# Performance work log

Hardware: AMD Instinct MI355X
Metric: run time of the kernel (lower is better)

The kernel has to match this reference:

```python
import jax, jax.numpy as jnp
import numpy as np

N_NODES = 50000
N_EDGES = 800000
IN_F, HID_F, OUT_F = 256, 128, 64
NEG_SLOPE = 0.2
EPS = 1e-16


def _aggregate_with_attention(x, src, tgt, a_w, a_b, num_nodes):
    # x: [N, d]; src/tgt: [E]; a_w: [2d]; a_b: [1]
    d = x.shape[-1]
    x_src = x[src]                                   # [E, d] gather
    # att(cat([x_src, x_tgt])) == x_src @ a_w[:d] + x_tgt @ a_w[d:] + b
    alpha = x_src @ a_w[:d] + x[tgt] @ a_w[d:] + a_b[0]   # [E]
    alpha = jnp.where(alpha >= 0, alpha, NEG_SLOPE * alpha)  # leaky_relu(0.2)
    # segment softmax over edges grouped by target node
    m = jax.ops.segment_max(alpha, tgt, num_segments=num_nodes)   # [N]
    e = jnp.exp(alpha - m[tgt])                                    # [E]
    s = jax.ops.segment_sum(e, tgt, num_segments=num_nodes)       # [N]
    alpha = e / (s[tgt] + EPS)                                     # [E]
    msgs = x_src * alpha[:, None]                                  # [E, d]
    return jax.ops.segment_sum(msgs, tgt, num_segments=num_nodes)  # [N, d]


def setup_inputs() -> dict:
    key = jax.random.key(0)
    ks = jax.random.split(key, 10)
    x = jax.random.normal(ks[0], (N_NODES, IN_F), dtype=jnp.float32)
    edge_index = jax.random.randint(ks[1], (2, N_EDGES), 0, N_NODES, dtype=jnp.int32)
    sc1 = 1.0 / np.sqrt(IN_F)
    sc2 = 1.0 / np.sqrt(HID_F)
    return {
        "x": x,
        "edge_index": edge_index,
        "W1": jax.random.normal(ks[2], (IN_F, HID_F), dtype=jnp.float32) * sc1,
        "b1": jax.random.normal(ks[3], (HID_F,), dtype=jnp.float32) * sc1,
        "a1_w": jax.random.normal(ks[4], (2 * HID_F,), dtype=jnp.float32) * sc2,
        "a1_b": jax.random.normal(ks[5], (1,), dtype=jnp.float32) * sc2,
        "W2": jax.random.normal(ks[6], (HID_F, OUT_F), dtype=jnp.float32) * sc2,
        "b2": jax.random.normal(ks[7], (OUT_F,), dtype=jnp.float32) * sc2,
        "a2_w": jax.random.normal(ks[8], (2 * OUT_F,), dtype=jnp.float32) * (1.0 / np.sqrt(OUT_F)),
        "a2_b": jax.random.normal(ks[9], (1,), dtype=jnp.float32) * (1.0 / np.sqrt(OUT_F)),
    }


def reference(x, edge_index, W1, b1, a1_w, a1_b, W2, b2, a2_w, a2_b):
    src, tgt = edge_index[0], edge_index[1]
    n = x.shape[0]
    # eval mode: dropout is identity
    h = jax.nn.elu(x @ W1 + b1)                           # [N, HID]
    h = _aggregate_with_attention(h, src, tgt, a1_w, a1_b, n)
    o = h @ W2 + b2                                        # [N, OUT]
    o = _aggregate_with_attention(o, src, tgt, a2_w, a2_b, n)
    return jax.nn.log_softmax(o, axis=-1)
```

## Files before the change

kernel.cpp:

```cpp
#include <hip/hip_runtime.h>

#define NN    50000
#define NE    800000
#define INF_  256
#define HIDF  128
#define OUTF  64
#define NBUCK 196
#define CAP   5120
#define CHUNK 2048
#define NPART1 ((NE + CHUNK - 1) / CHUNK)
#define NLIN1  ((NN + 63) / 64)
#define NPREP  160

typedef unsigned int uint;
typedef unsigned short ushort;
typedef __attribute__((ext_vector_type(8))) short short8;
typedef __attribute__((ext_vector_type(4))) float float4v;

__device__ __forceinline__ short f2bf(float f) {
    union { float f; unsigned u; } v; v.f = f;
    unsigned r = v.u + 0x7fffu + ((v.u >> 16) & 1u);
    return (short)(r >> 16);
}
__device__ __forceinline__ float bflo(uint u) {
    union { uint u; float f; } v; v.u = u << 16; return v.f;
}
__device__ __forceinline__ float bfhi(uint u) {
    union { uint u; float f; } v; v.u = u & 0xffff0000u; return v.f;
}

__device__ __forceinline__ int excl_scan256(int v, int* ws) {
    int lane = threadIdx.x & 63, wv = threadIdx.x >> 6;
    int x = v;
    #pragma unroll
    for (int o = 1; o < 64; o <<= 1) {
        int y = __shfl_up(x, o);
        if (lane >= o) x += y;
    }
    if (lane == 63) ws[wv] = x;
    __syncthreads();
    int add = 0;
    #pragma unroll
    for (int w = 0; w < 4; w++) add += (w < wv) ? ws[w] : 0;
    return x + add - v;
}

__global__ __launch_bounds__(256) void k_prep(const float* __restrict__ W1, const float* __restrict__ W2,
                                              short* __restrict__ W1f, short* __restrict__ W2f,
                                              int* __restrict__ bcur) {
    if (blockIdx.x == NPREP) {
        if (threadIdx.x < NBUCK) bcur[threadIdx.x] = 0;
        return;
    }
    int i = blockIdx.x * 256 + threadIdx.x;
    if (i < INF_ * HIDF) {
        int kk = i & 7, t = i >> 3;
        int m_l = t & 15, q = (t >> 4) & 3, s = t >> 6;
        int nb = s & 7, kc = s >> 3;
        int k = kc * 32 + q * 8 + kk, n = nb * 16 + m_l;
        W1f[i] = f2bf(W1[k * HIDF + n]);
    } else if (i < INF_ * HIDF + HIDF * OUTF) {
        int i2 = i - INF_ * HIDF;
        int kk = i2 & 7, t = i2 >> 3;
        int m_l = t & 15, q = (t >> 4) & 3, s = t >> 6;
        int nb = s & 3, kc = s >> 2;
        int k = kc * 32 + q * 8 + kk, n = nb * 16 + m_l;
        W2f[i2] = f2bf(W2[k * OUTF + n]);
    }
}


__global__ __launch_bounds__(256, 3) void k_f1(const int* __restrict__ src, const int* __restrict__ tgt,
                                               int* __restrict__ bcur, uint2* __restrict__ pairs,
                                               const float* __restrict__ X, const short* __restrict__ W1f,
                                               const float* __restrict__ b1, ushort* __restrict__ Hb,
                                               const float* __restrict__ a1w, float* __restrict__ s1s,
                                               float* __restrict__ s1t) {
    if (blockIdx.x < NPART1) {
        __shared__ int hist[NBUCK], lofs[NBUCK], cur[NBUCK], gstart[NBUCK];
        __shared__ int ws[4];
        __shared__ int ltgt[CHUNK], lsrc[CHUNK];
        int tid = threadIdx.x;
        for (int i = tid; i < NBUCK; i += 256) hist[i] = 0;
        __syncthreads();

        int base = blockIdx.x * CHUNK;
        int cnt = NE - base; if (cnt > CHUNK) cnt = CHUNK;

        int t_[8], s_[8];
        #pragma unroll
        for (int k = 0; k < 8; k++) {
            int idx = k * 256 + tid;
            if (idx < cnt) {
                int j = base + idx;
                t_[k] = tgt[j]; s_[k] = src[j];
                atomicAdd(&hist[t_[k] >> 8], 1);
            } else t_[k] = -1;
        }
        __syncthreads();

        int v = (tid < NBUCK) ? hist[tid] : 0;
        int excl = excl_scan256(v, ws);
        if (tid < NBUCK) {
            lofs[tid] = excl;
            cur[tid] = excl;
            gstart[tid] = atomicAdd(&bcur[tid], v);
        }
        __syncthreads();

        #pragma unroll
        for (int k = 0; k < 8; k++) {
            if (t_[k] >= 0) {
                int b = t_[k] >> 8;
                int pos = atomicAdd(&cur[b], 1);
                ltgt[pos] = t_[k]; lsrc[pos] = s_[k];
            }
        }
        __syncthreads();

        for (int j = tid; j < cnt; j += 256) {
            int tv = ltgt[j];
            int b = tv >> 8;
            int dst = gstart[b] + (j - lofs[b]);
            pairs[(size_t)b * CAP + dst] = make_uint2((uint)tv, (uint)lsrc[j]);
        }
        return;
    }
    int bid = blockIdx.x - NPART1;
    int w = threadIdx.x >> 6;
    int l = threadIdx.x & 63;
    int m_l = l & 15, q = l >> 4;
    int row0 = bid * 64 + w * 16;
    int rA0 = row0 + m_l;
    int rc0 = rA0 < NN ? rA0 : NN - 1;
    const float* pa0 = X + (size_t)rc0 * INF_ + q * 8;
    const short8* Bp = (const short8*)W1f;

    float4 xu[16];
    #pragma unroll
    for (int kc = 0; kc < 8; kc++) {
        xu[2 * kc]     = *(const float4*)(pa0 + kc * 32);
        xu[2 * kc + 1] = *(const float4*)(pa0 + kc * 32 + 4);
    }
    short8 af[8];
    #pragma unroll
    for (int kc = 0; kc < 8; kc++) {
        float4 u0 = xu[2 * kc], u1 = xu[2 * kc + 1];
        af[kc][0] = f2bf(u0.x); af[kc][1] = f2bf(u0.y); af[kc][2] = f2bf(u0.z); af[kc][3] = f2bf(u0.w);
        af[kc][4] = f2bf(u1.x); af[kc][5] = f2bf(u1.y); af[kc][6] = f2bf(u1.z); af[kc][7] = f2bf(u1.w);
    }

    float4v acc[8] = {};
    #pragma unroll
    for (int kc = 0; kc < 8; kc++) {
        #pragma unroll
        for (int n = 0; n < 8; n++) {
            short8 b = Bp[(kc * 8 + n) * 64 + l];
            acc[n] = __builtin_amdgcn_mfma_f32_16x16x32_bf16(af[kc], b, acc[n], 0, 0, 0);
        }
    }

    float vs_r[4] = {0.f, 0.f, 0.f, 0.f}, vt_r[4] = {0.f, 0.f, 0.f, 0.f};
    #pragma unroll
    for (int n = 0; n < 8; n++) {
        int col = n * 16 + m_l;
        float bias = b1[col];
        float aw0 = a1w[col], aw1 = a1w[HIDF + col];
        #pragma unroll
        for (int r = 0; r < 4; r++) {
            int row = row0 + q * 4 + r;
            float v = acc[n][r] + bias;
            v = v > 0.f ? v : expm1f(v);
            vs_r[r] += v * aw0; vt_r[r] += v * aw1;
            if (row < NN) Hb[(size_t)row * HIDF + col] = (ushort)f2bf(v);
        }
    }
    #pragma unroll
    for (int r = 0; r < 4; r++) {
        #pragma unroll
        for (int o = 1; o < 16; o <<= 1) {
            vs_r[r] += __shfl_xor(vs_r[r], o);
            vt_r[r] += __shfl_xor(vt_r[r], o);
        }
    }
    if (m_l == 0) {
        #pragma unroll
        for (int r = 0; r < 4; r++) {
            int row = row0 + q * 4 + r;
            if (row < NN) { s1s[row] = vs_r[r]; s1t[row] = vt_r[r]; }
        }
    }
}

__global__ __launch_bounds__(256) void k_part2(const int* __restrict__ bcur, const uint2* __restrict__ pairs,
                                               int* __restrict__ fsrc, int* __restrict__ nbeg,
                                               int* __restrict__ ncnt) {
    __shared__ int hist[256], cur[256];
    __shared__ int ws[4];
    int tid = threadIdx.x;
    int b = blockIdx.x;
    int cnt = __builtin_amdgcn_readfirstlane(bcur[b]);
    hist[tid] = 0;
    __syncthreads();

    const uint2* pb = pairs + (size_t)b * CAP;
    for (int j = tid; j < cnt; j += 256) {
        uint2 e = pb[j];
        atomicAdd(&hist[e.x & 255], 1);
    }
    __syncthreads();

    int v = hist[tid];
    int excl = excl_scan256(v, ws);
    int node = (b << 8) + tid;
    if (node < NN) { nbeg[node] = b * CAP + excl; ncnt[node] = v; }
    cur[tid] = excl;
    __syncthreads();

    for (int j = tid; j < cnt; j += 256) {
        uint2 e = pb[j];
        int pos = atomicAdd(&cur[e.x & 255], 1);
        fsrc[(size_t)b * CAP + pos] = (int)e.y;
    }
}

__global__ __launch_bounds__(256, 3) void k_linear2(const short* __restrict__ Hin, const short* __restrict__ W2f,
                                                    const float* __restrict__ b2, ushort* __restrict__ Ob,
                                                    const float* __restrict__ a2w, float* __restrict__ s2s,
                                                    float* __restrict__ s2t) {
    int w = threadIdx.x >> 6;
    int l = threadIdx.x & 63;
    int m_l = l & 15, q = l >> 4;
    int row0 = blockIdx.x * 64 + w * 16;
    int rA0 = row0 + m_l;
    int rc0 = rA0 < NN ? rA0 : NN - 1;
    const short* pa0 = Hin + (size_t)rc0 * HIDF + q * 8;
    const short8* Bp = (const short8*)W2f;

    short8 af[4];
    #pragma unroll
    for (int kc = 0; kc < 4; kc++) af[kc] = *(const short8*)(pa0 + kc * 32);

    float4v acc[4] = {};
    #pragma unroll
    for (int kc = 0; kc < 4; kc++) {
        #pragma unroll
        for (int n = 0; n < 4; n++) {
            short8 b = Bp[(kc * 4 + n) * 64 + l];
            acc[n] = __builtin_amdgcn_mfma_f32_16x16x32_bf16(af[kc], b, acc[n], 0, 0, 0);
        }
    }

    float vs_r[4] = {0.f, 0.f, 0.f, 0.f}, vt_r[4] = {0.f, 0.f, 0.f, 0.f};
    #pragma unroll
    for (int n = 0; n < 4; n++) {
        int col = n * 16 + m_l;
        float bias = b2[col];
        float aw0 = a2w[col], aw1 = a2w[OUTF + col];
        #pragma unroll
        for (int r = 0; r < 4; r++) {
            int row = row0 + q * 4 + r;
            float v = acc[n][r] + bias;
            vs_r[r] += v * aw0; vt_r[r] += v * aw1;
            if (row < NN) Ob[(size_t)row * OUTF + col] = (ushort)f2bf(v);
        }
    }
    #pragma unroll
    for (int r = 0; r < 4; r++) {
        #pragma unroll
        for (int o = 1; o < 16; o <<= 1) {
            vs_r[r] += __shfl_xor(vs_r[r], o);
            vt_r[r] += __shfl_xor(vt_r[r], o);
        }
    }
    if (m_l == 0) {
        #pragma unroll
        for (int r = 0; r < 4; r++) {
            int row = row0 + q * 4 + r;
            if (row < NN) { s2s[row] = vs_r[r]; s2t[row] = vt_r[r]; }
        }
    }
}


__global__ __launch_bounds__(256) void k_agg1f(const uint* __restrict__ Hb4, const int* __restrict__ nbeg,
                                               const int* __restrict__ ncnt, const int* __restrict__ fsrc,
                                               const float* __restrict__ ss, const float* __restrict__ st_,
                                               const float* __restrict__ ab, uint* __restrict__ Hagg4) {
    int wid  = (blockIdx.x * 256 + threadIdx.x) >> 6;
    int lane = threadIdx.x & 63;
    if (wid >= NN) return;
    int beg = __builtin_amdgcn_readfirstlane(nbeg[wid]);
    int deg = __builtin_amdgcn_readfirstlane(ncnt[wid]);
    int end = beg + deg;
    float bias = ab[0] + st_[wid];
    float ax = 0.f, ay = 0.f, bx = 0.f, by = 0.f;

    if (deg > 0 && deg <= 64) {
        int my_s = 0; float a = -INFINITY;
        if (lane < deg) {
            my_s = fsrc[beg + lane];
            float t = ss[my_s] + bias;
            a = t >= 0.f ? t : 0.2f * t;
        }
        float m = a;
        #pragma unroll
        for (int o = 32; o > 0; o >>= 1) m = fmaxf(m, __shfl_xor(m, o));
        float e = (lane < deg) ? __expf(a - m) : 0.f;
        float sum = e;
        #pragma unroll
        for (int o = 32; o > 0; o >>= 1) sum += __shfl_xor(sum, o);
        float p = e * (1.f / (sum + 1e-16f));
        for (int j = 0; j < deg; j += 8) {
            int sA[8]; float wA[8]; uint xA[8];
            #pragma unroll
            for (int u = 0; u < 8; u++) { sA[u] = __shfl(my_s, j + u); wA[u] = __shfl(p, j + u); }
            #pragma unroll
            for (int u = 0; u < 8; u++) xA[u] = Hb4[(size_t)sA[u] * 64 + lane];
            #pragma unroll
            for (int u = 0; u < 8; u += 2) {
                ax += wA[u] * bflo(xA[u]);         ay += wA[u] * bfhi(xA[u]);
                bx += wA[u + 1] * bflo(xA[u + 1]); by += wA[u + 1] * bfhi(xA[u + 1]);
            }
        }
    } else if (deg > 64) {
        float m = -INFINITY;
        for (int i = beg + lane; i < end; i += 64) {
            float t = ss[fsrc[i]] + bias;
            t = t >= 0.f ? t : 0.2f * t;
            m = fmaxf(m, t);
        }
        #pragma unroll
        for (int o = 32; o > 0; o >>= 1) m = fmaxf(m, __shfl_xor(m, o));
        float sum = 0.f;
        for (int i = beg + lane; i < end; i += 64) {
            float t = ss[fsrc[i]] + bias;
            t = t >= 0.f ? t : 0.2f * t;
            sum += __expf(t - m);
        }
        #pragma unroll
        for (int o = 32; o > 0; o >>= 1) sum += __shfl_xor(sum, o);
        float inv = 1.f / (sum + 1e-16f);
        for (int c = beg; c < end; c += 64) {
            int cnt = min(64, end - c);
            int my_s = 0; float p = 0.f;
            if (lane < cnt) {
                my_s = fsrc[c + lane];
                float t = ss[my_s] + bias;
                t = t >= 0.f ? t : 0.2f * t;
                p = __expf(t - m) * inv;
            }
            for (int j = 0; j < cnt; j += 4) {
                int s0 = __shfl(my_s, j),     s1 = __shfl(my_s, j + 1);
                int s2 = __shfl(my_s, j + 2), s3 = __shfl(my_s, j + 3);
                float w0 = __shfl(p, j),     w1 = __shfl(p, j + 1);
                float w2 = __shfl(p, j + 2), w3 = __shfl(p, j + 3);
                uint x0 = Hb4[(size_t)s0 * 64 + lane];
                uint x1 = Hb4[(size_t)s1 * 64 + lane];
                uint x2 = Hb4[(size_t)s2 * 64 + lane];
                uint x3 = Hb4[(size_t)s3 * 64 + lane];
                ax += w0 * bflo(x0); ay += w0 * bfhi(x0);
                bx += w1 * bflo(x1); by += w1 * bfhi(x1);
                ax += w2 * bflo(x2); ay += w2 * bfhi(x2);
                bx += w3 * bflo(x3); by += w3 * bfhi(x3);
            }
        }
    }
    float fx = ax + bx, fy = ay + by;
    uint outv = (uint)(ushort)f2bf(fx) | ((uint)(ushort)f2bf(fy) << 16);
    Hagg4[(size_t)wid * 64 + lane] = outv;
}

__global__ __launch_bounds__(256) void k_agg2f(const uint* __restrict__ Ob4, const int* __restrict__ nbeg,
                                               const int* __restrict__ ncnt, const int* __restrict__ fsrc,
                                               const float* __restrict__ ss, const float* __restrict__ st_,
                                               const float* __restrict__ ab, float* __restrict__ out) {
    int wid  = (blockIdx.x * 256 + threadIdx.x) >> 6;
    int lane = threadIdx.x & 63;
    if (wid >= NN) return;
    int half = lane >> 5, li = lane & 31;
    int beg = __builtin_amdgcn_readfirstlane(nbeg[wid]);
    int deg = __builtin_amdgcn_readfirstlane(ncnt[wid]);
    int end = beg + deg;
    float bias = ab[0] + st_[wid];
    float a0 = 0.f, a1 = 0.f;

    if (deg > 0 && deg <= 64) {
        int my_s = 0; float a = -INFINITY;
        if (lane < deg) {
            my_s = fsrc[beg + lane];
            float t = ss[my_s] + bias;
            a = t >= 0.f ? t : 0.2f * t;
        }
        float m = a;
        #pragma unroll
        for (int o = 32; o > 0; o >>= 1) m = fmaxf(m, __shfl_xor(m, o));
        float e = (lane < deg) ? __expf(a - m) : 0.f;
        float sum = e;
        #pragma unroll
        for (int o = 32; o > 0; o >>= 1) sum += __shfl_xor(sum, o);
        float p = e * (1.f / (sum + 1e-16f));
        for (int j = 0; j < deg; j += 8) {
            int e0 = j + half, e1 = j + 2 + half, e2 = j + 4 + half, e3 = j + 6 + half;
            int s0 = __shfl(my_s, e0), s1 = __shfl(my_s, e1);
            int s2 = __shfl(my_s, e2), s3 = __shfl(my_s, e3);
            float w0 = __shfl(p, e0), w1 = __shfl(p, e1);
            float w2 = __shfl(p, e2), w3 = __shfl(p, e3);
            uint x0 = Ob4[(size_t)s0 * 32 + li];
            uint x1 = Ob4[(size_t)s1 * 32 + li];
            uint x2 = Ob4[(size_t)s2 * 32 + li];
            uint x3 = Ob4[(size_t)s3 * 32 + li];
            a0 += w0 * bflo(x0); a1 += w0 * bfhi(x0);
            a0 += w1 * bflo(x1); a1 += w1 * bfhi(x1);
            a0 += w2 * bflo(x2); a1 += w2 * bfhi(x2);
            a0 += w3 * bflo(x3); a1 += w3 * bfhi(x3);
        }
    } else if (deg > 64) {
        float m = -INFINITY;
        for (int i = beg + lane; i < end; i += 64) {
            float t = ss[fsrc[i]] + bias;
            t = t >= 0.f ? t : 0.2f * t;
            m = fmaxf(m, t);
        }
        #pragma unroll
        for (int o = 32; o > 0; o >>= 1) m = fmaxf(m, __shfl_xor(m, o));
        float sum = 0.f;
        for (int i = beg + lane; i < end; i += 64) {
            float t = ss[fsrc[i]] + bias;
            t = t >= 0.f ? t : 0.2f * t;
            sum += __expf(t - m);
        }
        #pragma unroll
        for (int o = 32; o > 0; o >>= 1) sum += __shfl_xor(sum, o);
        float inv = 1.f / (sum + 1e-16f);
        for (int c = beg; c < end; c += 64) {
            int cnt = min(64, end - c);
            int my_s = 0; float p = 0.f;
            if (lane < cnt) {
                my_s = fsrc[c + lane];
                float t = ss[my_s] + bias;
                t = t >= 0.f ? t : 0.2f * t;
                p = __expf(t - m) * inv;
            }
            for (int j = 0; j < cnt; j += 4) {
                int e0 = j + half, e1 = j + 2 + half;
                int s0 = __shfl(my_s, e0), s1 = __shfl(my_s, e1);
                float w0 = __shfl(p, e0), w1 = __shfl(p, e1);
                uint x0 = Ob4[(size_t)s0 * 32 + li];
                uint x1 = Ob4[(size_t)s1 * 32 + li];
                a0 += w0 * bflo(x0); a1 += w0 * bfhi(x0);
                a0 += w1 * bflo(x1); a1 += w1 * bfhi(x1);
            }
        }
    }
    a0 += __shfl_xor(a0, 32);
    a1 += __shfl_xor(a1, 32);
    float mx = fmaxf(a0, a1);
    #pragma unroll
    for (int o = 16; o > 0; o >>= 1) mx = fmaxf(mx, __shfl_xor(mx, o));
    float es = __expf(a0 - mx) + __expf(a1 - mx);
    #pragma unroll
    for (int o = 16; o > 0; o >>= 1) es += __shfl_xor(es, o);
    float lg = __logf(es);
    if (half == 0) {
        float2 r; r.x = a0 - mx - lg; r.y = a1 - mx - lg;
        ((float2*)out)[(size_t)wid * 32 + li] = r;
    }
}


extern "C" void kernel_launch(void* const* d_in, const int* in_sizes, int n_in,
                              void* d_out, int out_size, void* d_ws, size_t ws_size,
                              hipStream_t stream) {
    const float* X   = (const float*)d_in[0];
    const int*   ei  = (const int*)d_in[1];
    const float* W1  = (const float*)d_in[2];
    const float* b1  = (const float*)d_in[3];
    const float* a1w = (const float*)d_in[4];
    const float* a1b = (const float*)d_in[5];
    const float* W2  = (const float*)d_in[6];
    const float* b2  = (const float*)d_in[7];
    const float* a2w = (const float*)d_in[8];
    const float* a2b = (const float*)d_in[9];
    const int* src = ei;
    const int* tgt = ei + NE;

    char* p = (char*)d_ws;
    size_t off = 0;
    auto alloc = [&](size_t bytes) -> char* {
        char* r = p + off;
        off = (off + bytes + 255) & ~(size_t)255;
        return r;
    };
    ushort* Hb    = (ushort*)alloc((size_t)NN * HIDF * 2);
    ushort* Hagg  = (ushort*)alloc((size_t)NN * HIDF * 2);
    ushort* Ob    = (ushort*)alloc((size_t)NN * OUTF * 2);
    short* W1f    = (short*)alloc((size_t)INF_ * HIDF * 2);
    short* W2f    = (short*)alloc((size_t)HIDF * OUTF * 2);
    float* s1s    = (float*)alloc((size_t)NN * 4);
    float* s1t    = (float*)alloc((size_t)NN * 4);
    float* s2s    = (float*)alloc((size_t)NN * 4);
    float* s2t    = (float*)alloc((size_t)NN * 4);
    int*   bcur   = (int*)alloc((size_t)NBUCK * 4);
    uint2* pairs  = (uint2*)alloc((size_t)NBUCK * CAP * 8);
    int*   fsrc   = (int*)alloc((size_t)NBUCK * CAP * 4);
    int*   nbeg   = (int*)alloc((size_t)NN * 4);
    int*   ncnt   = (int*)alloc((size_t)NN * 4);

    k_prep   <<<NPREP + 1, 256, 0, stream>>>(W1, W2, W1f, W2f, bcur);
    k_f1     <<<NPART1 + NLIN1, 256, 0, stream>>>(src, tgt, bcur, pairs,
                                                  X, W1f, b1, Hb, a1w, s1s, s1t);
    k_part2  <<<NBUCK, 256, 0, stream>>>(bcur, pairs, fsrc, nbeg, ncnt);
    k_agg1f  <<<NN / 4, 256, 0, stream>>>((const uint*)Hb, nbeg, ncnt, fsrc, s1s, s1t, a1b, (uint*)Hagg);
    k_linear2<<<NLIN1, 256, 0, stream>>>((const short*)Hagg, W2f, b2, Ob, a2w, s2s, s2t);
    k_agg2f  <<<NN / 4, 256, 0, stream>>>((const uint*)Ob, nbeg, ncnt, fsrc, s2s, s2t, a2b, (float*)d_out);
}
```

Before: 212.0 us.

## Stage X tile through LDS as bf16 and widen gather unroll to 16

The linear-layer part of k_f1 now loads the 64-row X tile with coalesced float4 reads, converts it to bf16 and stores it in padded shared memory (unioned with the partition scratch). MFMA A-fragments are then read from LDS instead of being held as 64 floats of strided global loads per lane. This aims to improve load coalescing and cut register pressure, and the launch_bounds occupancy hint is dropped. Separately, the aggregation loop for low-degree nodes gathers 16 neighbours per iteration instead of 8 to keep more loads in flight, at the cost of more registers and extra shuffles for padded lanes.

```diff
diff --git a/kernel.cpp b/kernel.cpp
--- a/kernel.cpp
+++ b/kernel.cpp
@@ -11,6 +11,7 @@
 #define NPART1 ((NE + CHUNK - 1) / CHUNK)
 #define NLIN1  ((NN + 63) / 64)
 #define NPREP  160
+#define XLD   264
 
 typedef unsigned int uint;
 typedef unsigned short ushort;
@@ -70,18 +71,26 @@
 }
 
 
-__global__ __launch_bounds__(256, 3) void k_f1(const int* __restrict__ src, const int* __restrict__ tgt,
-                                               int* __restrict__ bcur, uint2* __restrict__ pairs,
-                                               const float* __restrict__ X, const short* __restrict__ W1f,
-                                               const float* __restrict__ b1, ushort* __restrict__ Hb,
-                                               const float* __restrict__ a1w, float* __restrict__ s1s,
-                                               float* __restrict__ s1t) {
+struct P1Mem {
+    int hist[NBUCK], lofs[NBUCK], cur[NBUCK], gstart[NBUCK];
+    int ws[4];
+    int ltgt[CHUNK], lsrc[CHUNK];
+};
+union SMem {
+    P1Mem p1;
+    ushort xs[64][XLD];
+};
+
+__global__ __launch_bounds__(256) void k_f1(const int* __restrict__ src, const int* __restrict__ tgt,
+                                            int* __restrict__ bcur, uint2* __restrict__ pairs,
+                                            const float* __restrict__ X, const short* __restrict__ W1f,
+                                            const float* __restrict__ b1, ushort* __restrict__ Hb,
+                                            const float* __restrict__ a1w, float* __restrict__ s1s,
+                                            float* __restrict__ s1t) {
+    __shared__ SMem sm;
     if (blockIdx.x < NPART1) {
-        __shared__ int hist[NBUCK], lofs[NBUCK], cur[NBUCK], gstart[NBUCK];
-        __shared__ int ws[4];
-        __shared__ int ltgt[CHUNK], lsrc[CHUNK];
         int tid = threadIdx.x;
-        for (int i = tid; i < NBUCK; i += 256) hist[i] = 0;
+        for (int i = tid; i < NBUCK; i += 256) sm.p1.hist[i] = 0;
         __syncthreads();
 
         int base = blockIdx.x * CHUNK;
@@ -94,17 +103,17 @@
             if (idx < cnt) {
                 int j = base + idx;
                 t_[k] = tgt[j]; s_[k] = src[j];
-                atomicAdd(&hist[t_[k] >> 8], 1);
+                atomicAdd(&sm.p1.hist[t_[k] >> 8], 1);
             } else t_[k] = -1;
         }
         __syncthreads();
 
-        int v = (tid < NBUCK) ? hist[tid] : 0;
-        int excl = excl_scan256(v, ws);
+        int v = (tid < NBUCK) ? sm.p1.hist[tid] : 0;
+        int excl = excl_scan256(v, sm.p1.ws);
         if (tid < NBUCK) {
-            lofs[tid] = excl;
-            cur[tid] = excl;
-            gstart[tid] = atomicAdd(&bcur[tid], v);
+            sm.p1.lofs[tid] = excl;
+            sm.p1.cur[tid] = excl;
+            sm.p1.gstart[tid] = atomicAdd(&bcur[tid], v);
         }
         __syncthreads();
 
@@ -112,51 +121,52 @@
         for (int k = 0; k < 8; k++) {
             if (t_[k] >= 0) {
                 int b = t_[k] >> 8;
-                int pos = atomicAdd(&cur[b], 1);
-                ltgt[pos] = t_[k]; lsrc[pos] = s_[k];
+                int pos = atomicAdd(&sm.p1.cur[b], 1);
+                sm.p1.ltgt[pos] = t_[k]; sm.p1.lsrc[pos] = s_[k];
             }
         }
         __syncthreads();
 
         for (int j = tid; j < cnt; j += 256) {
-            int tv = ltgt[j];
+            int tv = sm.p1.ltgt[j];
             int b = tv >> 8;
-            int dst = gstart[b] + (j - lofs[b]);
-            pairs[(size_t)b * CAP + dst] = make_uint2((uint)tv, (uint)lsrc[j]);
+            int dst = sm.p1.gstart[b] + (j - sm.p1.lofs[b]);
+            pairs[(size_t)b * CAP + dst] = make_uint2((uint)tv, (uint)sm.p1.lsrc[j]);
         }
         return;
     }
     int bid = blockIdx.x - NPART1;
-    int w = threadIdx.x >> 6;
-    int l = threadIdx.x & 63;
+    int tid = threadIdx.x;
+
+    #pragma unroll
+    for (int it = 0; it < 16; it++) {
+        int flat = it * 1024 + tid * 4;
+        int row = flat >> 8, col = flat & 255;
+        int grow = bid * 64 + row;
+        float4 v = make_float4(0.f, 0.f, 0.f, 0.f);
+        if (grow < NN) v = *(const float4*)(X + (size_t)grow * INF_ + col);
+        uint2 pk;
+        pk.x = (uint)(ushort)f2bf(v.x) | ((uint)(ushort)f2bf(v.y) << 16);
+        pk.y = (uint)(ushort)f2bf(v.z) | ((uint)(ushort)f2bf(v.w) << 16);
+        *(uint2*)&sm.xs[row][col] = pk;
+    }
+    __syncthreads();
+
+    int w = tid >> 6;
+    int l = tid & 63;
     int m_l = l & 15, q = l >> 4;
     int row0 = bid * 64 + w * 16;
-    int rA0 = row0 + m_l;
-    int rc0 = rA0 < NN ? rA0 : NN - 1;
-    const float* pa0 = X + (size_t)rc0 * INF_ + q * 8;
     const short8* Bp = (const short8*)W1f;
-
-    float4 xu[16];
+    const ushort* xr = sm.xs[w * 16 + m_l];
+
+    float4v acc[8] = {};
     #pragma unroll
     for (int kc = 0; kc < 8; kc++) {
-        xu[2 * kc]     = *(const float4*)(pa0 + kc * 32);
-        xu[2 * kc + 1] = *(const float4*)(pa0 + kc * 32 + 4);
-    }
-    short8 af[8];
-    #pragma unroll
-    for (int kc = 0; kc < 8; kc++) {
-        float4 u0 = xu[2 * kc], u1 = xu[2 * kc + 1];
-        af[kc][0] = f2bf(u0.x); af[kc][1] = f2bf(u0.y); af[kc][2] = f2bf(u0.z); af[kc][3] = f2bf(u0.w);
-        af[kc][4] = f2bf(u1.x); af[kc][5] = f2bf(u1.y); af[kc][6] = f2bf(u1.z); af[kc][7] = f2bf(u1.w);
-    }
-
-    float4v acc[8] = {};
-    #pragma unroll
-    for (int kc = 0; kc < 8; kc++) {
+        short8 a0 = *(const short8*)(xr + kc * 32 + q * 8);
         #pragma unroll
         for (int n = 0; n < 8; n++) {
             short8 b = Bp[(kc * 8 + n) * 64 + l];
-            acc[n] = __builtin_amdgcn_mfma_f32_16x16x32_bf16(af[kc], b, acc[n], 0, 0, 0);
+            acc[n] = __builtin_amdgcn_mfma_f32_16x16x32_bf16(a0, b, acc[n], 0, 0, 0);
         }
     }
 
@@ -311,14 +321,14 @@
         #pragma unroll
         for (int o = 32; o > 0; o >>= 1) sum += __shfl_xor(sum, o);
         float p = e * (1.f / (sum + 1e-16f));
-        for (int j = 0; j < deg; j += 8) {
-            int sA[8]; float wA[8]; uint xA[8];
+        for (int j = 0; j < deg; j += 16) {
+            int sA[16]; float wA[16]; uint xA[16];
             #pragma unroll
-            for (int u = 0; u < 8; u++) { sA[u] = __shfl(my_s, j + u); wA[u] = __shfl(p, j + u); }
+            for (int u = 0; u < 16; u++) { sA[u] = __shfl(my_s, j + u); wA[u] = __shfl(p, j + u); }
             #pragma unroll
-            for (int u = 0; u < 8; u++) xA[u] = Hb4[(size_t)sA[u] * 64 + lane];
+            for (int u = 0; u < 16; u++) xA[u] = Hb4[(size_t)sA[u] * 64 + lane];
             #pragma unroll
-            for (int u = 0; u < 8; u += 2) {
+            for (int u = 0; u < 16; u += 2) {
                 ax += wA[u] * bflo(xA[u]);         ay += wA[u] * bfhi(xA[u]);
                 bx += wA[u + 1] * bflo(xA[u + 1]); by += wA[u + 1] * bfhi(xA[u + 1]);
             }
```

After: 214.5 us. No clear change (+1.2%).
